# Optimization experiments

Measured on AMD Instinct MI355X. Metric: run time of the kernel, lower is better.

## Reference

```python
import jax, jax.numpy as jnp
import numpy as np

TEMPERATURE = 0.1
BASE_TEMPERATURE = 0.1
COS_EPS = 1e-8  # torch.nn.CosineSimilarity default eps
BSZ, N_VIEWS, C = 8192, 1, 256
NUM_CLASSES = 1000


def setup_inputs() -> dict:
    key = jax.random.key(0)
    k1, k2 = jax.random.split(key)
    features = jax.random.normal(k1, (BSZ, N_VIEWS, C), dtype=jnp.float32)
    # int32 used (jax default x64 disabled); values are class ids in [0, NUM_CLASSES)
    labels = jax.random.randint(k2, (BSZ, N_VIEWS), 0, NUM_CLASSES, dtype=jnp.int32)
    return {"features": features, "labels": labels}


def reference(features, labels):
    # features: [bsz, n_views=1, C]; n_views==1 is the only shape-consistent case
    n = features.shape[0] * features.shape[1]
    f = features.reshape(n, -1)                       # contrast_feature == anchor_feature, [N, C]
    lab = labels.reshape(-1)                          # [N]

    # SupCon mask: mask_{ij} = 1 if same class
    mask = (lab[:, None] == lab[None, :]).astype(jnp.float32)   # [N, N]
    perfect_logit = jnp.where(mask == 1, 1.0, -1.0)

    # cosine similarity via L2-normalize + GEMM (same math as broadcasted CosineSimilarity)
    norms = jnp.linalg.norm(f, axis=-1, keepdims=True)
    fn = f / jnp.maximum(norms, COS_EPS)              # [N, C]
    logits = jnp.matmul(fn, fn.T) / TEMPERATURE       # [N, N]

    # logits_mask: ones with zeroed diagonal (exclude self-contrast)
    logits_mask = 1.0 - jnp.eye(n, dtype=jnp.float32)
    pos_mask = mask * logits_mask

    # faithful (unshifted) masked log-sum-exp, as in cal_log_prob
    denom = jnp.sum(jnp.exp(logits) * logits_mask, axis=1, keepdims=True)
    log_prob = logits - jnp.log(denom)                # [N, N]

    mean_log_prob_pos = jnp.sum(pos_mask * log_prob, axis=1) / (jnp.sum(pos_mask, axis=1) + 1e-6)
    loss = jnp.mean(-(TEMPERATURE / BASE_TEMPERATURE) * mean_log_prob_pos)
    return (loss, logits, perfect_logit)
```

## Files before the change

kernel.cpp:

```cpp
#include <hip/hip_runtime.h>
#include <hip/hip_bf16.h>

#define N 8192
#define C 256
#define NCLS 1000

typedef __bf16 bf16x8 __attribute__((ext_vector_type(8)));
typedef float floatx4 __attribute__((ext_vector_type(4)));

__device__ __forceinline__ void gload_lds16(const void* g, void* l) {
    __builtin_amdgcn_global_load_lds(
        (const __attribute__((address_space(1))) void*)g,
        (__attribute__((address_space(3))) void*)l, 16, 0, 0);
}

__device__ __forceinline__ unsigned short f2bf(float x) {
    union { float f; unsigned int u; } a; a.f = x;
    unsigned int u = a.u;
    unsigned int r = (u + 0x7fffu + ((u >> 16) & 1u)) >> 16;
    return (unsigned short)r;
}

__global__ __launch_bounds__(256) void k_norm(const float* __restrict__ f,
                                              unsigned short* __restrict__ fnb) {
    int wid = threadIdx.x >> 6, lane = threadIdx.x & 63;
    int row = blockIdx.x * 4 + wid;
    const float4* fr = (const float4*)(f + (size_t)row * C);
    float4 v = fr[lane];
    float ss = v.x * v.x + v.y * v.y + v.z * v.z + v.w * v.w;
    #pragma unroll
    for (int m = 1; m < 64; m <<= 1) ss += __shfl_xor(ss, m, 64);
    float scale = 1.0f / fmaxf(sqrtf(ss), 1e-8f);
    ushort4 o;
    o.x = f2bf(v.x * scale); o.y = f2bf(v.y * scale);
    o.z = f2bf(v.z * scale); o.w = f2bf(v.w * scale);
    ((ushort4*)(fnb + (size_t)row * C))[lane] = o;
}

__global__ __launch_bounds__(1024) void k_hist(const int* __restrict__ lab,
                                               int* __restrict__ cnt) {
    __shared__ int bins[NCLS];
    for (int i = threadIdx.x; i < NCLS; i += 1024) bins[i] = 0;
    __syncthreads();
    for (int i = threadIdx.x; i < N; i += 1024) atomicAdd(&bins[lab[i]], 1);
    __syncthreads();
    for (int i = threadIdx.x; i < NCLS; i += 1024) cnt[i] = bins[i];
}

__global__ __launch_bounds__(256) void k_gemm(
    const unsigned short* __restrict__ fnb, const int* __restrict__ lab,
    float* __restrict__ logits, float* __restrict__ perfect,
    float* __restrict__ Ssum, float* __restrict__ Psum) {
    __shared__ __align__(16) unsigned short As[128 * 32];
    __shared__ __align__(16) unsigned short Bs[128 * 32];
    __shared__ int Lr[128], Lc[128];

    const int t = threadIdx.x;
    const int wid = t >> 6, lane = t & 63;
    const int waveM = wid >> 1, waveN = wid & 1;
    const int quad = lane >> 4, l15 = lane & 15;
    const int rowBase = blockIdx.y * 128;
    const int colBase = blockIdx.x * 128;

    if (t < 128) Lr[t] = lab[rowBase + t];
    else         Lc[t - 128] = lab[colBase + (t - 128)];

    floatx4 acc[4][4] = {};

    const int srow = wid * 16 + (lane >> 2);
    const int scol = (lane & 3) * 8;
    const unsigned short* gA = fnb + (size_t)(rowBase + srow) * C + scol;
    const unsigned short* gB = fnb + (size_t)(colBase + srow) * C + scol;
    char* asb = (char*)As + wid * 1024;
    char* bsb = (char*)Bs + wid * 1024;

    for (int kb = 0; kb < C; kb += 32) {
        __syncthreads();
        gload_lds16(gA + kb,           asb);
        gload_lds16(gA + kb + 64 * C,  asb + 4096);
        gload_lds16(gB + kb,           bsb);
        gload_lds16(gB + kb + 64 * C,  bsb + 4096);
        __syncthreads();
        bf16x8 a[4], b[4];
        #pragma unroll
        for (int i = 0; i < 4; ++i) {
            a[i] = *(const bf16x8*)&As[(waveM * 64 + i * 16 + l15) * 32 + quad * 8];
            b[i] = *(const bf16x8*)&Bs[(waveN * 64 + i * 16 + l15) * 32 + quad * 8];
        }
        #pragma unroll
        for (int i = 0; i < 4; ++i)
            #pragma unroll
            for (int j = 0; j < 4; ++j)
                acc[i][j] = __builtin_amdgcn_mfma_f32_16x16x32_bf16(a[i], b[j], acc[i][j], 0, 0, 0);
    }

    const float invT = 10.0f;
    #pragma unroll
    for (int i = 0; i < 4; ++i) {
        #pragma unroll
        for (int r = 0; r < 4; ++r) {
            int lrow = waveM * 64 + i * 16 + quad * 4 + r;
            int row = rowBase + lrow;
            int labr = Lr[lrow];
            float eSum = 0.f, pSum = 0.f;
            #pragma unroll
            for (int j = 0; j < 4; ++j) {
                int lcol = waveN * 64 + j * 16 + l15;
                int col = colBase + lcol;
                float v = acc[i][j][r] * invT;
                size_t off = (size_t)row * N + col;
                logits[off] = v;
                bool same = (labr == Lc[lcol]);
                perfect[off] = same ? 1.0f : -1.0f;
                if (row != col) {
                    eSum += __expf(v);
                    if (same) pSum += v;
                }
            }
            #pragma unroll
            for (int m = 1; m < 16; m <<= 1) {
                eSum += __shfl_xor(eSum, m, 64);
                pSum += __shfl_xor(pSum, m, 64);
            }
            if (l15 == 0) {
                atomicAdd(&Ssum[row], eSum);
                if (pSum != 0.0f) atomicAdd(&Psum[row], pSum);
            }
        }
    }
}

__global__ __launch_bounds__(1024) void k_loss(
    const float* __restrict__ S, const float* __restrict__ P,
    const int* __restrict__ lab, const int* __restrict__ cnt,
    float* __restrict__ out) {
    float sum = 0.f;
    for (int i = threadIdx.x; i < N; i += 1024) {
        float Ki = (float)(cnt[lab[i]] - 1);
        float term = (P[i] - Ki * logf(S[i])) / (Ki + 1e-6f);
        sum += term;
    }
    #pragma unroll
    for (int m = 1; m < 64; m <<= 1) sum += __shfl_xor(sum, m, 64);
    __shared__ float wsum[16];
    int wid = threadIdx.x >> 6, lane = threadIdx.x & 63;
    if (lane == 0) wsum[wid] = sum;
    __syncthreads();
    if (threadIdx.x == 0) {
        float tot = 0.f;
        #pragma unroll
        for (int i = 0; i < 16; ++i) tot += wsum[i];
        out[0] = -tot / (float)N;
    }
}

extern "C" void kernel_launch(void* const* d_in, const int* in_sizes, int n_in,
                              void* d_out, int out_size, void* d_ws, size_t ws_size,
                              hipStream_t stream) {
    const float* f = (const float*)d_in[0];
    const int* lab = (const int*)d_in[1];
    float* out = (float*)d_out;
    float* logits = out + 1;
    float* perfect = out + 1 + (size_t)N * N;

    unsigned short* fnb = (unsigned short*)d_ws;
    float* Ssum = (float*)((char*)d_ws + (size_t)N * C * 2);
    float* Psum = Ssum + N;
    int* cnt = (int*)(Psum + N);

    hipMemsetAsync(Ssum, 0, 2 * N * sizeof(float), stream);
    k_norm<<<N / 4, 256, 0, stream>>>(f, fnb);
    k_hist<<<1, 1024, 0, stream>>>(lab, cnt);
    k_gemm<<<dim3(64, 64), 256, 0, stream>>>(fnb, lab, logits, perfect, Ssum, Psum);
    k_loss<<<1, 1024, 0, stream>>>(Ssum, Psum, lab, cnt, out);
}
```

Before: 667.5 us.

## Exploit Gram matrix symmetry: compute upper-triangle tiles and mirror-store transposes

Since the logits matrix is symmetric, blocks below the diagonal now exit early. Each upper-triangle block writes both its tile and the transposed tile, and adds column-wise exp and positive sums into the row accumulators for the mirrored rows. This roughly halves the MFMA and operand-load work. Stores become nontemporal, and the transposed stores go out as 4-wide vectors. Output write volume is unchanged, so the gain is limited if the kernel is bound by store bandwidth, and half the launched blocks do no work.

```diff
diff --git a/kernel.cpp b/kernel.cpp
--- a/kernel.cpp
+++ b/kernel.cpp
@@ -51,6 +51,10 @@
     const unsigned short* __restrict__ fnb, const int* __restrict__ lab,
     float* __restrict__ logits, float* __restrict__ perfect,
     float* __restrict__ Ssum, float* __restrict__ Psum) {
+    const int bx = blockIdx.x, by = blockIdx.y;
+    if (bx < by) return;
+    const bool diag = (bx == by);
+
     __shared__ __align__(16) unsigned short As[128 * 32];
     __shared__ __align__(16) unsigned short Bs[128 * 32];
     __shared__ int Lr[128], Lc[128];
@@ -59,8 +63,8 @@
     const int wid = t >> 6, lane = t & 63;
     const int waveM = wid >> 1, waveN = wid & 1;
     const int quad = lane >> 4, l15 = lane & 15;
-    const int rowBase = blockIdx.y * 128;
-    const int colBase = blockIdx.x * 128;
+    const int rowBase = by * 128;
+    const int colBase = bx * 128;
 
     if (t < 128) Lr[t] = lab[rowBase + t];
     else         Lc[t - 128] = lab[colBase + (t - 128)];
@@ -95,6 +99,9 @@
     }
 
     const float invT = 10.0f;
+    float colS[4] = {0.f, 0.f, 0.f, 0.f};
+    float colP[4] = {0.f, 0.f, 0.f, 0.f};
+
     #pragma unroll
     for (int i = 0; i < 4; ++i) {
         #pragma unroll
@@ -102,29 +109,71 @@
             int lrow = waveM * 64 + i * 16 + quad * 4 + r;
             int row = rowBase + lrow;
             int labr = Lr[lrow];
-            float eSum = 0.f, pSum = 0.f;
+            float eS = 0.f, pS = 0.f;
             #pragma unroll
             for (int j = 0; j < 4; ++j) {
                 int lcol = waveN * 64 + j * 16 + l15;
                 int col = colBase + lcol;
                 float v = acc[i][j][r] * invT;
                 size_t off = (size_t)row * N + col;
-                logits[off] = v;
                 bool same = (labr == Lc[lcol]);
-                perfect[off] = same ? 1.0f : -1.0f;
-                if (row != col) {
-                    eSum += __expf(v);
-                    if (same) pSum += v;
+                __builtin_nontemporal_store(v, logits + off);
+                __builtin_nontemporal_store(same ? 1.0f : -1.0f, perfect + off);
+                if (!diag || row != col) {
+                    float e = __expf(v);
+                    eS += e;
+                    if (same) pS += v;
+                    if (!diag) {
+                        colS[j] += e;
+                        if (same) colP[j] += v;
+                    }
                 }
             }
             #pragma unroll
             for (int m = 1; m < 16; m <<= 1) {
-                eSum += __shfl_xor(eSum, m, 64);
-                pSum += __shfl_xor(pSum, m, 64);
+                eS += __shfl_xor(eS, m, 64);
+                pS += __shfl_xor(pS, m, 64);
             }
             if (l15 == 0) {
-                atomicAdd(&Ssum[row], eSum);
-                if (pSum != 0.0f) atomicAdd(&Psum[row], pSum);
+                atomicAdd(&Ssum[row], eS);
+                if (pS != 0.0f) atomicAdd(&Psum[row], pS);
+            }
+        }
+    }
+
+    if (!diag) {
+        #pragma unroll
+        for (int i = 0; i < 4; ++i) {
+            int lr0 = waveM * 64 + i * 16 + quad * 4;
+            int tcol0 = rowBase + lr0;
+            int la0 = Lr[lr0 + 0], la1 = Lr[lr0 + 1];
+            int la2 = Lr[lr0 + 2], la3 = Lr[lr0 + 3];
+            #pragma unroll
+            for (int j = 0; j < 4; ++j) {
+                int lcol = waveN * 64 + j * 16 + l15;
+                int trow = colBase + lcol;
+                int labc = Lc[lcol];
+                floatx4 lv, pv;
+                lv[0] = acc[i][j][0] * invT; lv[1] = acc[i][j][1] * invT;
+                lv[2] = acc[i][j][2] * invT; lv[3] = acc[i][j][3] * invT;
+                pv[0] = (la0 == labc) ? 1.0f : -1.0f;
+                pv[1] = (la1 == labc) ? 1.0f : -1.0f;
+                pv[2] = (la2 == labc) ? 1.0f : -1.0f;
+                pv[3] = (la3 == labc) ? 1.0f : -1.0f;
+                size_t off = (size_t)trow * N + tcol0;
+                __builtin_nontemporal_store(lv, (floatx4*)(logits + off));
+                __builtin_nontemporal_store(pv, (floatx4*)(perfect + off));
+            }
+        }
+        #pragma unroll
+        for (int j = 0; j < 4; ++j) {
+            float cs = colS[j], cp = colP[j];
+            cs += __shfl_xor(cs, 16, 64); cs += __shfl_xor(cs, 32, 64);
+            cp += __shfl_xor(cp, 16, 64); cp += __shfl_xor(cp, 32, 64);
+            if (quad == 0) {
+                int col = colBase + waveN * 64 + j * 16 + l15;
+                atomicAdd(&Ssum[col], cs);
+                if (cp != 0.0f) atomicAdd(&Psum[col], cp);
             }
         }
     }
```

Measured after the change: 1.080 ms. 1.62x slower.

## Split perfect-logit writer into own kernel; row-strip GEMM with LDS-staged coalesced stores

Applied to the files above, without the earlier changes.

Moves the perfect-logit mask into a separate streaming kernel that writes full rows with nontemporal float4 stores. The GEMM becomes a 16-row strip per block: the A fragments stay in registers and B is read directly from global memory. Each 1024-column chunk is staged in LDS and written out as coalesced nontemporal float4 rows. Row sums are reduced within the block, so the atomics and the memset go away. The cost is far less reuse of B, since every block streams the whole normalized matrix from global or L2 memory, and the number of blocks drops to 512.

```diff
diff --git a/kernel.cpp b/kernel.cpp
--- a/kernel.cpp
+++ b/kernel.cpp
@@ -7,12 +7,6 @@
 
 typedef __bf16 bf16x8 __attribute__((ext_vector_type(8)));
 typedef float floatx4 __attribute__((ext_vector_type(4)));
-
-__device__ __forceinline__ void gload_lds16(const void* g, void* l) {
-    __builtin_amdgcn_global_load_lds(
-        (const __attribute__((address_space(1))) void*)g,
-        (__attribute__((address_space(3))) void*)l, 16, 0, 0);
-}
 
 __device__ __forceinline__ unsigned short f2bf(float x) {
     union { float f; unsigned int u; } a; a.f = x;
@@ -47,86 +41,122 @@
     for (int i = threadIdx.x; i < NCLS; i += 1024) cnt[i] = bins[i];
 }
 
+__global__ __launch_bounds__(256) void k_perfect(const int* __restrict__ lab,
+                                                 float* __restrict__ perfect) {
+    __shared__ __align__(16) int labs[N];
+    const int t = threadIdx.x;
+    #pragma unroll
+    for (int p = 0; p < 8; ++p) {
+        int idx = (p * 256 + t) * 4;
+        *(int4*)&labs[idx] = *(const int4*)(lab + idx);
+    }
+    __syncthreads();
+    const int row0 = blockIdx.x * 8;
+    int lr[8];
+    #pragma unroll
+    for (int rr = 0; rr < 8; ++rr) lr[rr] = labs[row0 + rr];
+    #pragma unroll
+    for (int p = 0; p < 8; ++p) {
+        int c = (p * 256 + t) * 4;
+        int4 lv = *(const int4*)&labs[c];
+        #pragma unroll
+        for (int rr = 0; rr < 8; ++rr) {
+            floatx4 pv;
+            pv[0] = (lv.x == lr[rr]) ? 1.0f : -1.0f;
+            pv[1] = (lv.y == lr[rr]) ? 1.0f : -1.0f;
+            pv[2] = (lv.z == lr[rr]) ? 1.0f : -1.0f;
+            pv[3] = (lv.w == lr[rr]) ? 1.0f : -1.0f;
+            __builtin_nontemporal_store(pv,
+                (floatx4*)(perfect + (size_t)(row0 + rr) * N + c));
+        }
+    }
+}
+
+#define CH 1024
+#define STRIDE 1036
+
 __global__ __launch_bounds__(256) void k_gemm(
     const unsigned short* __restrict__ fnb, const int* __restrict__ lab,
-    float* __restrict__ logits, float* __restrict__ perfect,
+    float* __restrict__ logits,
     float* __restrict__ Ssum, float* __restrict__ Psum) {
-    __shared__ __align__(16) unsigned short As[128 * 32];
-    __shared__ __align__(16) unsigned short Bs[128 * 32];
-    __shared__ int Lr[128], Lc[128];
+    __shared__ __align__(16) float stage[16 * STRIDE];
+    __shared__ float SrowW[4][16], ProwW[4][16];
+    __shared__ int Lr[16];
 
     const int t = threadIdx.x;
     const int wid = t >> 6, lane = t & 63;
-    const int waveM = wid >> 1, waveN = wid & 1;
     const int quad = lane >> 4, l15 = lane & 15;
-    const int rowBase = blockIdx.y * 128;
-    const int colBase = blockIdx.x * 128;
-
-    if (t < 128) Lr[t] = lab[rowBase + t];
-    else         Lc[t - 128] = lab[colBase + (t - 128)];
-
-    floatx4 acc[4][4] = {};
-
-    const int srow = wid * 16 + (lane >> 2);
-    const int scol = (lane & 3) * 8;
-    const unsigned short* gA = fnb + (size_t)(rowBase + srow) * C + scol;
-    const unsigned short* gB = fnb + (size_t)(colBase + srow) * C + scol;
-    char* asb = (char*)As + wid * 1024;
-    char* bsb = (char*)Bs + wid * 1024;
-
-    for (int kb = 0; kb < C; kb += 32) {
+    const int row0 = blockIdx.x * 16;
+
+    if (t < 16) Lr[t] = lab[row0 + t];
+
+    bf16x8 a[8];
+    const unsigned short* arow = fnb + (size_t)(row0 + l15) * C + quad * 8;
+    #pragma unroll
+    for (int ks = 0; ks < 8; ++ks) a[ks] = *(const bf16x8*)(arow + ks * 32);
+
+    __syncthreads();
+    int labr[4];
+    #pragma unroll
+    for (int r = 0; r < 4; ++r) labr[r] = Lr[quad * 4 + r];
+
+    const float invT = 10.0f;
+    float eS[4] = {0.f, 0.f, 0.f, 0.f};
+    float pS[4] = {0.f, 0.f, 0.f, 0.f};
+
+    for (int ch = 0; ch < 8; ++ch) {
+        const int cwave = wid * 256;
+        #pragma unroll 4
+        for (int tl = 0; tl < 16; ++tl) {
+            const int cloc = cwave + tl * 16;
+            const int colAbs = ch * CH + cloc + l15;
+            const unsigned short* brow =
+                fnb + (size_t)colAbs * C + quad * 8;
+            floatx4 acc = {};
+            #pragma unroll
+            for (int ks = 0; ks < 8; ++ks) {
+                bf16x8 b = *(const bf16x8*)(brow + ks * 32);
+                acc = __builtin_amdgcn_mfma_f32_16x16x32_bf16(a[ks], b, acc, 0, 0, 0);
+            }
+            int labc = lab[colAbs];
+            #pragma unroll
+            for (int r = 0; r < 4; ++r) {
+                float v = acc[r] * invT;
+                int rowAbs = row0 + quad * 4 + r;
+                if (colAbs != rowAbs) {
+                    eS[r] += __expf(v);
+                    if (labc == labr[r]) pS[r] += v;
+                }
+                stage[(quad * 4 + r) * STRIDE + cloc + l15] = v;
+            }
+        }
         __syncthreads();
-        gload_lds16(gA + kb,           asb);
-        gload_lds16(gA + kb + 64 * C,  asb + 4096);
-        gload_lds16(gB + kb,           bsb);
-        gload_lds16(gB + kb + 64 * C,  bsb + 4096);
+        float* gbase = logits + (size_t)row0 * N + ch * CH;
+        #pragma unroll
+        for (int row = 0; row < 16; ++row) {
+            floatx4 w = *(const floatx4*)&stage[row * STRIDE + t * 4];
+            __builtin_nontemporal_store(w,
+                (floatx4*)(gbase + (size_t)row * N + t * 4));
+        }
         __syncthreads();
-        bf16x8 a[4], b[4];
-        #pragma unroll
-        for (int i = 0; i < 4; ++i) {
-            a[i] = *(const bf16x8*)&As[(waveM * 64 + i * 16 + l15) * 32 + quad * 8];
-            b[i] = *(const bf16x8*)&Bs[(waveN * 64 + i * 16 + l15) * 32 + quad * 8];
-        }
-        #pragma unroll
-        for (int i = 0; i < 4; ++i)
-            #pragma unroll
-            for (int j = 0; j < 4; ++j)
-                acc[i][j] = __builtin_amdgcn_mfma_f32_16x16x32_bf16(a[i], b[j], acc[i][j], 0, 0, 0);
-    }
-
-    const float invT = 10.0f;
-    #pragma unroll
-    for (int i = 0; i < 4; ++i) {
-        #pragma unroll
-        for (int r = 0; r < 4; ++r) {
-            int lrow = waveM * 64 + i * 16 + quad * 4 + r;
-            int row = rowBase + lrow;
-            int labr = Lr[lrow];
-            float eSum = 0.f, pSum = 0.f;
-            #pragma unroll
-            for (int j = 0; j < 4; ++j) {
-                int lcol = waveN * 64 + j * 16 + l15;
-                int col = colBase + lcol;
-                float v = acc[i][j][r] * invT;
-                size_t off = (size_t)row * N + col;
-                logits[off] = v;
-                bool same = (labr == Lc[lcol]);
-                perfect[off] = same ? 1.0f : -1.0f;
-                if (row != col) {
-                    eSum += __expf(v);
-                    if (same) pSum += v;
-                }
-            }
-            #pragma unroll
-            for (int m = 1; m < 16; m <<= 1) {
-                eSum += __shfl_xor(eSum, m, 64);
-                pSum += __shfl_xor(pSum, m, 64);
-            }
-            if (l15 == 0) {
-                atomicAdd(&Ssum[row], eSum);
-                if (pSum != 0.0f) atomicAdd(&Psum[row], pSum);
-            }
-        }
+    }
+
+    #pragma unroll
+    for (int r = 0; r < 4; ++r) {
+        float e = eS[r], p = pS[r];
+        e += __shfl_xor(e, 1, 64); e += __shfl_xor(e, 2, 64);
+        e += __shfl_xor(e, 4, 64); e += __shfl_xor(e, 8, 64);
+        p += __shfl_xor(p, 1, 64); p += __shfl_xor(p, 2, 64);
+        p += __shfl_xor(p, 4, 64); p += __shfl_xor(p, 8, 64);
+        if (l15 == 0) {
+            SrowW[wid][quad * 4 + r] = e;
+            ProwW[wid][quad * 4 + r] = p;
+        }
+    }
+    __syncthreads();
+    if (t < 16) {
+        Ssum[row0 + t] = SrowW[0][t] + SrowW[1][t] + SrowW[2][t] + SrowW[3][t];
+        Psum[row0 + t] = ProwW[0][t] + ProwW[1][t] + ProwW[2][t] + ProwW[3][t];
     }
 }
 
@@ -168,9 +198,9 @@
     float* Psum = Ssum + N;
     int* cnt = (int*)(Psum + N);
 
-    hipMemsetAsync(Ssum, 0, 2 * N * sizeof(float), stream);
     k_norm<<<N / 4, 256, 0, stream>>>(f, fnb);
     k_hist<<<1, 1024, 0, stream>>>(lab, cnt);
-    k_gemm<<<dim3(64, 64), 256, 0, stream>>>(fnb, lab, logits, perfect, Ssum, Psum);
+    k_perfect<<<N / 8, 256, 0, stream>>>(lab, perfect);
+    k_gemm<<<N / 16, 256, 0, stream>>>(fnb, lab, logits, Ssum, Psum);
     k_loss<<<1, 1024, 0, stream>>>(Ssum, Psum, lab, cnt, out);
 }
```

Result: slower. 777.6 us (+16.5%).
